# Kernel tuning notes

Measured on AMD Instinct MI355X. Metric: run time of the kernel, lower is better.

Reference implementation:

```python
import jax, jax.numpy as jnp
import numpy as np

DIM = 1024
HEADS = 16
DIM_HEAD = 64
INNER = HEADS * DIM_HEAD
EPS_NORM = 1e-12  # F.normalize eps
LN_EPS = 1e-5     # torch F.layer_norm default eps


def setup_inputs() -> dict:
    key = jax.random.key(0)
    ks = jax.random.split(key, 6)
    x = jax.random.normal(ks[0], (8, 1024, DIM), dtype=jnp.float32)
    ln_gamma = jnp.ones((DIM,), jnp.float32)
    q_gamma = jnp.ones((HEADS, 1, DIM_HEAD), jnp.float32)
    k_gamma = jnp.ones((HEADS, 1, DIM_HEAD), jnp.float32)
    # nn.Linear default init ~ U(-1/sqrt(fan_in), 1/sqrt(fan_in))
    w_qkv = jax.random.uniform(ks[1], (DIM, 3 * INNER), jnp.float32, -1.0, 1.0) / np.sqrt(DIM)
    w_out = jax.random.uniform(ks[2], (INNER, DIM), jnp.float32, -1.0, 1.0) / np.sqrt(INNER)
    return {"x": x, "ln_gamma": ln_gamma, "q_gamma": q_gamma, "k_gamma": k_gamma,
            "w_qkv": w_qkv, "w_out": w_out}


def _layer_norm(x, gamma):
    mu = jnp.mean(x, axis=-1, keepdims=True)
    var = jnp.var(x, axis=-1, keepdims=True)
    return (x - mu) * jax.lax.rsqrt(var + LN_EPS) * gamma  # beta is zeros buffer


def _rms(x, gamma):
    # F.normalize(x, dim=-1) * sqrt(d) * gamma
    n = jnp.linalg.norm(x, axis=-1, keepdims=True)
    normed = x / jnp.maximum(n, EPS_NORM)
    return normed * (DIM_HEAD ** 0.5) * gamma


def reference(x, ln_gamma, q_gamma, k_gamma, w_qkv, w_out):
    b, n, _ = x.shape
    h, d = HEADS, DIM_HEAD
    xn = _layer_norm(x, ln_gamma)
    qkv = xn @ w_qkv  # [b, n, 3*inner]
    q, k, v = jnp.split(qkv, 3, axis=-1)
    # b n (h d) -> b h n d
    to_heads = lambda t: t.reshape(b, n, h, d).transpose(0, 2, 1, 3)
    q, k, v = to_heads(q), to_heads(k), to_heads(v)
    q = _rms(q, q_gamma)
    k = _rms(k, k_gamma)
    dots = jnp.einsum('bhid,bhjd->bhij', q, k)  # no extra scale (scale baked into RMSNorm)
    attn = jax.nn.softmax(dots, axis=-1)
    out = jnp.einsum('bhij,bhjd->bhid', attn, v)
    out = out.transpose(0, 2, 1, 3).reshape(b, n, h * d)
    return out @ w_out
```

## Files before the change

### kernel.cpp

```cpp
#include <hip/hip_runtime.h>
#include <hip/hip_bf16.h>
#include <math.h>

#define DIMX   1024
#define HEADS  16
#define DH     64
#define NB     8
#define NSEQ   1024
#define ROWS   (NB * NSEQ)
#define QKVW   (3 * DIMX)
#define LOG2E  1.44269504088896f

typedef _Float16 half8 __attribute__((ext_vector_type(8)));
typedef _Float16 half4 __attribute__((ext_vector_type(4)));
typedef float floatx4 __attribute__((ext_vector_type(4)));

#define GLD_LDS16(gptr, lptr) __builtin_amdgcn_global_load_lds( \
    (const __attribute__((address_space(1))) void*)(gptr),      \
    (__attribute__((address_space(3))) void*)(lptr), 16, 0, 0)

__device__ __forceinline__ float fexp2(float x) {
#if __has_builtin(__builtin_amdgcn_exp2f)
    return __builtin_amdgcn_exp2f(x);
#else
    return __expf(x * 0.69314718056f);
#endif
}

__global__ __launch_bounds__(256) void ln_kernel(const float* __restrict__ x,
                                                 const float* __restrict__ gamma,
                                                 _Float16* __restrict__ xn) {
    int row = blockIdx.x;
    const float* xr = x + (size_t)row * DIMX;
    _Float16* xo = xn + (size_t)row * DIMX;
    int t = threadIdx.x;

    float4 v = ((const float4*)xr)[t];
    float s  = v.x + v.y + v.z + v.w;
    float ss = v.x*v.x + v.y*v.y + v.z*v.z + v.w*v.w;

    #pragma unroll
    for (int o = 32; o > 0; o >>= 1) {
        s  += __shfl_down(s, o);
        ss += __shfl_down(ss, o);
    }
    __shared__ float sbuf[4], ssbuf[4];
    int lane = t & 63, wid = t >> 6;
    if (lane == 0) { sbuf[wid] = s; ssbuf[wid] = ss; }
    __syncthreads();
    if (t == 0) {
        float a = 0.f, b2 = 0.f;
        for (int i = 0; i < 4; i++) { a += sbuf[i]; b2 += ssbuf[i]; }
        sbuf[0] = a; ssbuf[0] = b2;
    }
    __syncthreads();
    float mean = sbuf[0] * (1.0f / DIMX);
    float var  = ssbuf[0] * (1.0f / DIMX) - mean * mean;
    float rstd = rsqrtf(var + 1e-5f);

    float4 g = ((const float4*)gamma)[t];
    half4 o;
    o.x = (_Float16)((v.x - mean) * rstd * g.x);
    o.y = (_Float16)((v.y - mean) * rstd * g.y);
    o.z = (_Float16)((v.z - mean) * rstd * g.z);
    o.w = (_Float16)((v.w - mean) * rstd * g.w);
    *(half4*)(xo + t * 4) = o;
}

__global__ __launch_bounds__(256) void wtrans2(const float* __restrict__ Wq,
                                               const float* __restrict__ Wo,
                                               _Float16* __restrict__ WqT,
                                               _Float16* __restrict__ WoT) {
    __shared__ float tile[32][33];
    const float* W; _Float16* WT; int N, n0;
    if (blockIdx.x < 96) { W = Wq; WT = WqT; N = QKVW; n0 = blockIdx.x * 32; }
    else                 { W = Wo; WT = WoT; N = DIMX; n0 = (blockIdx.x - 96) * 32; }
    int k0 = blockIdx.y * 32;
    int tx = threadIdx.x & 31, ty = threadIdx.x >> 5;
    #pragma unroll
    for (int i = 0; i < 32; i += 8)
        tile[ty + i][tx] = W[(size_t)(k0 + ty + i) * N + n0 + tx];
    __syncthreads();
    #pragma unroll
    for (int i = 0; i < 32; i += 8)
        WT[(size_t)(n0 + ty + i) * 1024 + k0 + tx] = (_Float16)tile[tx][ty + i];
}

__global__ __launch_bounds__(256) void hgemm_qkv(const _Float16* __restrict__ A,
                                                 const _Float16* __restrict__ BT,
                                                 const float* __restrict__ qg,
                                                 const float* __restrict__ kg,
                                                 _Float16* __restrict__ qf,
                                                 _Float16* __restrict__ kf,
                                                 _Float16* __restrict__ vraw) {
    __shared__ _Float16 As[128 * 64];
    __shared__ _Float16 Bs[128 * 64];
    const int K = DIMX;

    int t = threadIdx.x;
    int wave = t >> 6, lane = t & 63;
    int quad = lane >> 4, l16 = lane & 15;
    int wm = (wave >> 1) * 64;
    int wn = (wave & 1) * 64;
    size_t m0 = (size_t)blockIdx.y * 128, n0 = (size_t)blockIdx.x * 128;

    floatx4 acc[4][4] = {};

    int sr = t >> 3, sg = t & 7;
    int swz = sg ^ (sr & 7);
    const _Float16* ag = A  + (m0 + sr) * (size_t)K + swz * 8;
    const _Float16* bg = BT + (n0 + sr) * (size_t)K + swz * 8;
    char* lA = (char*)As + (t >> 6) * 1024;
    char* lB = (char*)Bs + (t >> 6) * 1024;

    for (int k0 = 0; k0 < K; k0 += 64) {
        #pragma unroll
        for (int i = 0; i < 4; i++) {
            GLD_LDS16(ag + (size_t)(i * 32) * K + k0, lA + i * 4096);
            GLD_LDS16(bg + (size_t)(i * 32) * K + k0, lB + i * 4096);
        }
        __syncthreads();

        half8 af[2][4], bf[2][4];
        #pragma unroll
        for (int kk = 0; kk < 2; kk++) {
            #pragma unroll
            for (int mf = 0; mf < 4; mf++)
                af[kk][mf] = *(const half8*)&As[(wm + mf * 16 + l16) * 64
                                 + (((kk * 4 + quad) ^ (l16 & 7)) * 8)];
            #pragma unroll
            for (int nf = 0; nf < 4; nf++)
                bf[kk][nf] = *(const half8*)&Bs[(wn + nf * 16 + l16) * 64
                                 + (((kk * 4 + quad) ^ (l16 & 7)) * 8)];
        }

        #pragma unroll
        for (int kk = 0; kk < 2; kk++)
            #pragma unroll
            for (int mf = 0; mf < 4; mf++)
                #pragma unroll
                for (int nf = 0; nf < 4; nf++)
                    acc[mf][nf] = __builtin_amdgcn_mfma_f32_16x16x32_f16(
                        bf[kk][nf], af[kk][mf], acc[mf][nf], 0, 0, 0);
        __syncthreads();
    }

    int which = (int)(n0 >> 10);
    int nloc  = ((int)n0 & 1023) + wn;
    int h = nloc >> 6;
    const float* g = (which == 0) ? qg : kg;
    float emul = (which == 0) ? LOG2E : 1.0f;
    _Float16* dstbuf = (which == 0) ? qf : (which == 1) ? kf : vraw;

    #pragma unroll
    for (int mf = 0; mf < 4; mf++) {
        size_t tok = m0 + wm + mf * 16 + l16;
        int b = (int)(tok >> 10), ntk = (int)(tok & 1023);
        _Float16* dst = dstbuf + (((size_t)(b * 16 + h)) * 1024 + ntk) * 64;
        if (which < 2) {
            float ss = 0.f;
            #pragma unroll
            for (int nf = 0; nf < 4; nf++)
                #pragma unroll
                for (int r = 0; r < 4; r++) ss += acc[mf][nf][r] * acc[mf][nf][r];
            ss += __shfl_xor(ss, 16);
            ss += __shfl_xor(ss, 32);
            float scale = 8.0f * emul / fmaxf(sqrtf(ss), 1e-12f);
            #pragma unroll
            for (int nf = 0; nf < 4; nf++) {
                half4 p;
                #pragma unroll
                for (int r = 0; r < 4; r++)
                    p[r] = (_Float16)(acc[mf][nf][r] * scale *
                                      g[h * 64 + nf * 16 + quad * 4 + r]);
                *(half4*)(dst + nf * 16 + quad * 4) = p;
            }
        } else {
            #pragma unroll
            for (int nf = 0; nf < 4; nf++) {
                half4 p;
                #pragma unroll
                for (int r = 0; r < 4; r++) p[r] = (_Float16)acc[mf][nf][r];
                *(half4*)(dst + nf * 16 + quad * 4) = p;
            }
        }
    }
}

__global__ __launch_bounds__(256) void vtrans(const _Float16* __restrict__ vraw,
                                              _Float16* __restrict__ vt) {
    __shared__ _Float16 tile[64][72];
    int blk = blockIdx.x;
    int bh = blk >> 4, nt = blk & 15;
    int t = threadIdx.x;
    int r = t >> 2, cg = t & 3;

    const _Float16* src = vraw + ((size_t)bh * 1024 + nt * 64 + r) * 64 + cg * 16;
    half8 v0 = *(const half8*)src;
    half8 v1 = *(const half8*)(src + 8);
    #pragma unroll
    for (int j = 0; j < 8; j++) tile[cg * 16 + j][r] = v0[j];
    #pragma unroll
    for (int j = 0; j < 8; j++) tile[cg * 16 + 8 + j][r] = v1[j];
    __syncthreads();
    int d = t >> 2, ng = t & 3;
    half8 w0, w1;
    #pragma unroll
    for (int j = 0; j < 8; j++) { w0[j] = tile[d][ng * 16 + j]; w1[j] = tile[d][ng * 16 + 8 + j]; }
    _Float16* vdst = vt + ((size_t)blk * 64 + d) * 64 + ng * 16;
    *(half8*)vdst = w0;
    *(half8*)(vdst + 8) = w1;
}

__global__ __launch_bounds__(256) void flash_kernel(const _Float16* __restrict__ qf,
                                                    const _Float16* __restrict__ kf,
                                                    const _Float16* __restrict__ vt,
                                                    _Float16* __restrict__ obuf) {
    __shared__ _Float16 Ks[64 * 64];
    __shared__ _Float16 VTs[64 * 64];
    __shared__ _Float16 Ps[4][16][68];

    int t = threadIdx.x;
    int wave = t >> 6, lane = t & 63;
    int quad = lane >> 4, l16 = lane & 15;
    int bh = blockIdx.x >> 3, qt = blockIdx.x & 7;

    const _Float16* qb = qf + ((size_t)bh * 1024 + qt * 128) * 64;
    const _Float16* kb = kf + (size_t)bh * 65536;
    const _Float16* vb = vt + (size_t)bh * 65536;

    half8 aq[2][2];
    #pragma unroll
    for (int st = 0; st < 2; st++) {
        const _Float16* qrow = qb + (wave * 32 + st * 16 + l16) * 64;
        aq[st][0] = *(const half8*)(qrow + quad * 8);
        aq[st][1] = *(const half8*)(qrow + 32 + quad * 8);
    }

    floatx4 o[2][4] = {};
    float m_i[2] = {-INFINITY, -INFINITY};
    float l_i[2] = {0.f, 0.f};

    int sr = t >> 3;
    int sg = t & 7;
    int swz = sg ^ (sr & 7);
    char* lK = (char*)Ks  + (t >> 6) * 1024;
    char* lV = (char*)VTs + (t >> 6) * 1024;

    for (int kt = 0; kt < 16; kt++) {
        const _Float16* kbt = kb + (size_t)kt * 64 * 64;
        const _Float16* vbt = vb + (size_t)kt * 64 * 64;
        #pragma unroll
        for (int i = 0; i < 2; i++) {
            GLD_LDS16(kbt + (i * 32 + sr) * 64 + swz * 8, lK + i * 4096);
            GLD_LDS16(vbt + (i * 32 + sr) * 64 + swz * 8, lV + i * 4096);
        }
        __syncthreads();

        #pragma unroll
        for (int st = 0; st < 2; st++) {
            floatx4 sc[4] = {};
            #pragma unroll
            for (int kc = 0; kc < 2; kc++) {
                #pragma unroll
                for (int nf = 0; nf < 4; nf++) {
                    half8 ak = *(const half8*)&Ks[(nf * 16 + l16) * 64
                                    + (((kc * 4 + quad) ^ (l16 & 7)) * 8)];
                    sc[nf] = __builtin_amdgcn_mfma_f32_16x16x32_f16(
                        ak, aq[st][kc], sc[nf], 0, 0, 0);
                }
            }

            float mx = sc[0][0];
            #pragma unroll
            for (int nf = 0; nf < 4; nf++)
                #pragma unroll
                for (int r = 0; r < 4; r++) mx = fmaxf(mx, sc[nf][r]);
            mx = fmaxf(mx, __shfl_xor(mx, 16));
            mx = fmaxf(mx, __shfl_xor(mx, 32));
            if (mx > m_i[st]) {
                float alpha = fexp2(m_i[st] - mx);
                l_i[st] *= alpha;
                #pragma unroll
                for (int nf = 0; nf < 4; nf++) o[st][nf] *= alpha;
                m_i[st] = mx;
            }
            float mcur = m_i[st];
            float psum = 0.f;
            #pragma unroll
            for (int nf = 0; nf < 4; nf++)
                #pragma unroll
                for (int r = 0; r < 4; r++) {
                    float p = fexp2(sc[nf][r] - mcur);
                    sc[nf][r] = p;
                    psum += p;
                }
            l_i[st] += psum;

            #pragma unroll
            for (int nf = 0; nf < 4; nf++) {
                half4 p4;
                #pragma unroll
                for (int r = 0; r < 4; r++) p4[r] = (_Float16)sc[nf][r];
                *(half4*)&Ps[wave][l16][nf * 16 + quad * 4] = p4;
            }

            #pragma unroll
            for (int kc = 0; kc < 2; kc++) {
                half4 p0 = *(const half4*)&Ps[wave][l16][kc * 32 + quad * 8];
                half4 p1 = *(const half4*)&Ps[wave][l16][kc * 32 + quad * 8 + 4];
                half8 bp;
                #pragma unroll
                for (int j = 0; j < 4; j++) { bp[j] = p0[j]; bp[4 + j] = p1[j]; }
                #pragma unroll
                for (int nf = 0; nf < 4; nf++) {
                    half8 av = *(const half8*)&VTs[(nf * 16 + l16) * 64
                                    + (((kc * 4 + quad) ^ (l16 & 7)) * 8)];
                    o[st][nf] = __builtin_amdgcn_mfma_f32_16x16x32_f16(
                        av, bp, o[st][nf], 0, 0, 0);
                }
            }
        }
        __syncthreads();
    }

    int b = bh >> 4, h = bh & 15;
    #pragma unroll
    for (int st = 0; st < 2; st++) {
        float lsum = l_i[st];
        lsum += __shfl_xor(lsum, 16);
        lsum += __shfl_xor(lsum, 32);
        float inv = 1.0f / lsum;
        size_t row = (size_t)b * NSEQ + qt * 128 + wave * 32 + st * 16 + l16;
        #pragma unroll
        for (int nf = 0; nf < 4; nf++) {
            half4 o4;
            #pragma unroll
            for (int r = 0; r < 4; r++) o4[r] = (_Float16)(o[st][nf][r] * inv);
            *(half4*)(obuf + row * 1024 + h * 64 + nf * 16 + quad * 4) = o4;
        }
    }
}

__global__ __launch_bounds__(256) void hgemm_out(const _Float16* __restrict__ A,
                                                 const _Float16* __restrict__ BT,
                                                 float* __restrict__ C) {
    __shared__ _Float16 As[128 * 64];
    __shared__ _Float16 Bs[128 * 64];
    const int K = DIMX, N = DIMX;

    int t = threadIdx.x;
    int wave = t >> 6, lane = t & 63;
    int quad = lane >> 4, l16 = lane & 15;
    int wm = (wave >> 1) * 64, wn = (wave & 1) * 64;
    size_t m0 = (size_t)blockIdx.y * 128, n0 = (size_t)blockIdx.x * 128;

    floatx4 acc[4][4] = {};

    int sr = t >> 3, sg = t & 7;
    int swz = sg ^ (sr & 7);
    const _Float16* ag = A  + (m0 + sr) * (size_t)K + swz * 8;
    const _Float16* bg = BT + (n0 + sr) * (size_t)K + swz * 8;
    char* lA = (char*)As + (t >> 6) * 1024;
    char* lB = (char*)Bs + (t >> 6) * 1024;

    for (int k0 = 0; k0 < K; k0 += 64) {
        #pragma unroll
        for (int i = 0; i < 4; i++) {
            GLD_LDS16(ag + (size_t)(i * 32) * K + k0, lA + i * 4096);
            GLD_LDS16(bg + (size_t)(i * 32) * K + k0, lB + i * 4096);
        }
        __syncthreads();

        half8 af[2][4], bf[2][4];
        #pragma unroll
        for (int kk = 0; kk < 2; kk++) {
            #pragma unroll
            for (int mf = 0; mf < 4; mf++)
                af[kk][mf] = *(const half8*)&As[(wm + mf * 16 + l16) * 64
                                 + (((kk * 4 + quad) ^ (l16 & 7)) * 8)];
            #pragma unroll
            for (int nf = 0; nf < 4; nf++)
                bf[kk][nf] = *(const half8*)&Bs[(wn + nf * 16 + l16) * 64
                                 + (((kk * 4 + quad) ^ (l16 & 7)) * 8)];
        }

        #pragma unroll
        for (int kk = 0; kk < 2; kk++)
            #pragma unroll
            for (int mf = 0; mf < 4; mf++)
                #pragma unroll
                for (int nf = 0; nf < 4; nf++)
                    acc[mf][nf] = __builtin_amdgcn_mfma_f32_16x16x32_f16(
                        bf[kk][nf], af[kk][mf], acc[mf][nf], 0, 0, 0);
        __syncthreads();
    }

    #pragma unroll
    for (int mf = 0; mf < 4; mf++) {
        size_t tok = m0 + wm + mf * 16 + l16;
        #pragma unroll
        for (int nf = 0; nf < 4; nf++)
            *(floatx4*)(C + tok * N + n0 + wn + nf * 16 + quad * 4) = acc[mf][nf];
    }
}

extern "C" void kernel_launch(void* const* d_in, const int* in_sizes, int n_in,
                              void* d_out, int out_size, void* d_ws, size_t ws_size,
                              hipStream_t stream) {
    const float* x     = (const float*)d_in[0];
    const float* ln_g  = (const float*)d_in[1];
    const float* q_g   = (const float*)d_in[2];
    const float* k_g   = (const float*)d_in[3];
    const float* w_qkv = (const float*)d_in[4];
    const float* w_out = (const float*)d_in[5];
    float* out = (float*)d_out;

    char* base = (char*)d_ws;
    _Float16* xn    = (_Float16*)(base);
    _Float16* wqkvT = (_Float16*)(base + (16ull << 20));
    _Float16* woutT = (_Float16*)(base + (22ull << 20));
    _Float16* qf    = (_Float16*)(base + (24ull << 20));
    _Float16* kf    = (_Float16*)(base + (40ull << 20));
    _Float16* vraw  = (_Float16*)(base + (56ull << 20));
    _Float16* vt    = (_Float16*)(base + (72ull << 20));
    _Float16* obuf  = (_Float16*)(base + (88ull << 20));

    ln_kernel<<<ROWS, 256, 0, stream>>>(x, ln_g, xn);

    dim3 gt(128, 32);
    wtrans2<<<gt, 256, 0, stream>>>(w_qkv, w_out, wqkvT, woutT);

    dim3 g1(QKVW / 128, ROWS / 128);
    hgemm_qkv<<<g1, 256, 0, stream>>>(xn, wqkvT, q_g, k_g, qf, kf, vraw);

    vtrans<<<NB * HEADS * (NSEQ / 64), 256, 0, stream>>>(vraw, vt);

    flash_kernel<<<NB * HEADS * (NSEQ / 128), 256, 0, stream>>>(qf, kf, vt, obuf);

    dim3 g2(DIMX / 128, ROWS / 128);
    hgemm_out<<<g2, 256, 0, stream>>>(obuf, woutT, out);
}
```

Measured before the change: 270.6 us.

## Fuse LN with weight transpose, write V transposed in GEMM, double-buffer flash

Merges the layer-norm and weight-transpose kernels into one launch, and removes the separate V transpose kernel by having the QKV GEMM epilogue write V directly in transposed tile layout. The flash attention kernel now double-buffers its K/V tiles in LDS, prefetching the next tile while computing the current one, with one barrier per iteration. It also reorders block indexing so query tiles of the same head are spread across the grid, and adds a launch-bounds occupancy hint. The transposed V stores are strided scalar 2-byte writes, which may be poorly coalesced, and the doubled LDS footprint may limit occupancy.

```diff
diff --git a/kernel.cpp b/kernel.cpp
--- a/kernel.cpp
+++ b/kernel.cpp
@@ -27,63 +27,66 @@
 #endif
 }
 
-__global__ __launch_bounds__(256) void ln_kernel(const float* __restrict__ x,
-                                                 const float* __restrict__ gamma,
-                                                 _Float16* __restrict__ xn) {
-    int row = blockIdx.x;
-    const float* xr = x + (size_t)row * DIMX;
-    _Float16* xo = xn + (size_t)row * DIMX;
+__global__ __launch_bounds__(256) void lnw_kernel(const float* __restrict__ x,
+                                                  const float* __restrict__ gamma,
+                                                  const float* __restrict__ Wq,
+                                                  const float* __restrict__ Wo,
+                                                  _Float16* __restrict__ xn,
+                                                  _Float16* __restrict__ WqT,
+                                                  _Float16* __restrict__ WoT) {
+    __shared__ float tile[32][33];
+    __shared__ float sbuf[4], ssbuf[4];
     int t = threadIdx.x;
 
-    float4 v = ((const float4*)xr)[t];
-    float s  = v.x + v.y + v.z + v.w;
-    float ss = v.x*v.x + v.y*v.y + v.z*v.z + v.w*v.w;
-
-    #pragma unroll
-    for (int o = 32; o > 0; o >>= 1) {
-        s  += __shfl_down(s, o);
-        ss += __shfl_down(ss, o);
-    }
-    __shared__ float sbuf[4], ssbuf[4];
-    int lane = t & 63, wid = t >> 6;
-    if (lane == 0) { sbuf[wid] = s; ssbuf[wid] = ss; }
-    __syncthreads();
-    if (t == 0) {
-        float a = 0.f, b2 = 0.f;
-        for (int i = 0; i < 4; i++) { a += sbuf[i]; b2 += ssbuf[i]; }
-        sbuf[0] = a; ssbuf[0] = b2;
-    }
-    __syncthreads();
-    float mean = sbuf[0] * (1.0f / DIMX);
-    float var  = ssbuf[0] * (1.0f / DIMX) - mean * mean;
-    float rstd = rsqrtf(var + 1e-5f);
-
-    float4 g = ((const float4*)gamma)[t];
-    half4 o;
-    o.x = (_Float16)((v.x - mean) * rstd * g.x);
-    o.y = (_Float16)((v.y - mean) * rstd * g.y);
-    o.z = (_Float16)((v.z - mean) * rstd * g.z);
-    o.w = (_Float16)((v.w - mean) * rstd * g.w);
-    *(half4*)(xo + t * 4) = o;
-}
-
-__global__ __launch_bounds__(256) void wtrans2(const float* __restrict__ Wq,
-                                               const float* __restrict__ Wo,
-                                               _Float16* __restrict__ WqT,
-                                               _Float16* __restrict__ WoT) {
-    __shared__ float tile[32][33];
-    const float* W; _Float16* WT; int N, n0;
-    if (blockIdx.x < 96) { W = Wq; WT = WqT; N = QKVW; n0 = blockIdx.x * 32; }
-    else                 { W = Wo; WT = WoT; N = DIMX; n0 = (blockIdx.x - 96) * 32; }
-    int k0 = blockIdx.y * 32;
-    int tx = threadIdx.x & 31, ty = threadIdx.x >> 5;
-    #pragma unroll
-    for (int i = 0; i < 32; i += 8)
-        tile[ty + i][tx] = W[(size_t)(k0 + ty + i) * N + n0 + tx];
-    __syncthreads();
-    #pragma unroll
-    for (int i = 0; i < 32; i += 8)
-        WT[(size_t)(n0 + ty + i) * 1024 + k0 + tx] = (_Float16)tile[tx][ty + i];
+    if (blockIdx.x < ROWS) {
+        int row = blockIdx.x;
+        const float* xr = x + (size_t)row * DIMX;
+        _Float16* xo = xn + (size_t)row * DIMX;
+
+        float4 v = ((const float4*)xr)[t];
+        float s  = v.x + v.y + v.z + v.w;
+        float ss = v.x*v.x + v.y*v.y + v.z*v.z + v.w*v.w;
+        #pragma unroll
+        for (int o = 32; o > 0; o >>= 1) {
+            s  += __shfl_down(s, o);
+            ss += __shfl_down(ss, o);
+        }
+        int lane = t & 63, wid = t >> 6;
+        if (lane == 0) { sbuf[wid] = s; ssbuf[wid] = ss; }
+        __syncthreads();
+        if (t == 0) {
+            float a = 0.f, b2 = 0.f;
+            for (int i = 0; i < 4; i++) { a += sbuf[i]; b2 += ssbuf[i]; }
+            sbuf[0] = a; ssbuf[0] = b2;
+        }
+        __syncthreads();
+        float mean = sbuf[0] * (1.0f / DIMX);
+        float var  = ssbuf[0] * (1.0f / DIMX) - mean * mean;
+        float rstd = rsqrtf(var + 1e-5f);
+
+        float4 g = ((const float4*)gamma)[t];
+        half4 o;
+        o.x = (_Float16)((v.x - mean) * rstd * g.x);
+        o.y = (_Float16)((v.y - mean) * rstd * g.y);
+        o.z = (_Float16)((v.z - mean) * rstd * g.z);
+        o.w = (_Float16)((v.w - mean) * rstd * g.w);
+        *(half4*)(xo + t * 4) = o;
+    } else {
+        int idx = blockIdx.x - ROWS;
+        int bx = idx & 127, by = idx >> 7;
+        const float* W; _Float16* WT; int N, n0;
+        if (bx < 96) { W = Wq; WT = WqT; N = QKVW; n0 = bx * 32; }
+        else         { W = Wo; WT = WoT; N = DIMX; n0 = (bx - 96) * 32; }
+        int k0 = by * 32;
+        int tx = t & 31, ty = t >> 5;
+        #pragma unroll
+        for (int i = 0; i < 32; i += 8)
+            tile[ty + i][tx] = W[(size_t)(k0 + ty + i) * N + n0 + tx];
+        __syncthreads();
+        #pragma unroll
+        for (int i = 0; i < 32; i += 8)
+            WT[(size_t)(n0 + ty + i) * 1024 + k0 + tx] = (_Float16)tile[tx][ty + i];
+    }
 }
 
 __global__ __launch_bounds__(256) void hgemm_qkv(const _Float16* __restrict__ A,
@@ -92,7 +95,7 @@
                                                  const float* __restrict__ kg,
                                                  _Float16* __restrict__ qf,
                                                  _Float16* __restrict__ kf,
-                                                 _Float16* __restrict__ vraw) {
+                                                 _Float16* __restrict__ vt) {
     __shared__ _Float16 As[128 * 64];
     __shared__ _Float16 Bs[128 * 64];
     const int K = DIMX;
@@ -110,8 +113,8 @@
     int swz = sg ^ (sr & 7);
     const _Float16* ag = A  + (m0 + sr) * (size_t)K + swz * 8;
     const _Float16* bg = BT + (n0 + sr) * (size_t)K + swz * 8;
-    char* lA = (char*)As + (t >> 6) * 1024;
-    char* lB = (char*)Bs + (t >> 6) * 1024;
+    char* lA = (char*)As + wave * 1024;
+    char* lB = (char*)Bs + wave * 1024;
 
     for (int k0 = 0; k0 < K; k0 += 64) {
         #pragma unroll
@@ -148,16 +151,16 @@
     int which = (int)(n0 >> 10);
     int nloc  = ((int)n0 & 1023) + wn;
     int h = nloc >> 6;
-    const float* g = (which == 0) ? qg : kg;
-    float emul = (which == 0) ? LOG2E : 1.0f;
-    _Float16* dstbuf = (which == 0) ? qf : (which == 1) ? kf : vraw;
-
-    #pragma unroll
-    for (int mf = 0; mf < 4; mf++) {
-        size_t tok = m0 + wm + mf * 16 + l16;
-        int b = (int)(tok >> 10), ntk = (int)(tok & 1023);
-        _Float16* dst = dstbuf + (((size_t)(b * 16 + h)) * 1024 + ntk) * 64;
-        if (which < 2) {
+
+    if (which < 2) {
+        const float* g = (which == 0) ? qg : kg;
+        float emul = (which == 0) ? LOG2E : 1.0f;
+        _Float16* dstbuf = (which == 0) ? qf : kf;
+        #pragma unroll
+        for (int mf = 0; mf < 4; mf++) {
+            size_t tok = m0 + wm + mf * 16 + l16;
+            int b = (int)(tok >> 10), ntk = (int)(tok & 1023);
+            _Float16* dst = dstbuf + (((size_t)(b * 16 + h)) * 1024 + ntk) * 64;
             float ss = 0.f;
             #pragma unroll
             for (int nf = 0; nf < 4; nf++)
@@ -175,55 +178,37 @@
                                       g[h * 64 + nf * 16 + quad * 4 + r]);
                 *(half4*)(dst + nf * 16 + quad * 4) = p;
             }
-        } else {
-            #pragma unroll
-            for (int nf = 0; nf < 4; nf++) {
-                half4 p;
-                #pragma unroll
-                for (int r = 0; r < 4; r++) p[r] = (_Float16)acc[mf][nf][r];
-                *(half4*)(dst + nf * 16 + quad * 4) = p;
-            }
-        }
-    }
-}
-
-__global__ __launch_bounds__(256) void vtrans(const _Float16* __restrict__ vraw,
-                                              _Float16* __restrict__ vt) {
-    __shared__ _Float16 tile[64][72];
-    int blk = blockIdx.x;
-    int bh = blk >> 4, nt = blk & 15;
-    int t = threadIdx.x;
-    int r = t >> 2, cg = t & 3;
-
-    const _Float16* src = vraw + ((size_t)bh * 1024 + nt * 64 + r) * 64 + cg * 16;
-    half8 v0 = *(const half8*)src;
-    half8 v1 = *(const half8*)(src + 8);
-    #pragma unroll
-    for (int j = 0; j < 8; j++) tile[cg * 16 + j][r] = v0[j];
-    #pragma unroll
-    for (int j = 0; j < 8; j++) tile[cg * 16 + 8 + j][r] = v1[j];
-    __syncthreads();
-    int d = t >> 2, ng = t & 3;
-    half8 w0, w1;
-    #pragma unroll
-    for (int j = 0; j < 8; j++) { w0[j] = tile[d][ng * 16 + j]; w1[j] = tile[d][ng * 16 + 8 + j]; }
-    _Float16* vdst = vt + ((size_t)blk * 64 + d) * 64 + ng * 16;
-    *(half8*)vdst = w0;
-    *(half8*)(vdst + 8) = w1;
-}
-
-__global__ __launch_bounds__(256) void flash_kernel(const _Float16* __restrict__ qf,
-                                                    const _Float16* __restrict__ kf,
-                                                    const _Float16* __restrict__ vt,
-                                                    _Float16* __restrict__ obuf) {
-    __shared__ _Float16 Ks[64 * 64];
-    __shared__ _Float16 VTs[64 * 64];
+        }
+    } else {
+        #pragma unroll
+        for (int mf = 0; mf < 4; mf++) {
+            size_t tok = m0 + wm + mf * 16 + l16;
+            int b = (int)(tok >> 10), ntk = (int)(tok & 1023);
+            int nt = ntk >> 6;
+            _Float16* vd = vt + ((size_t)((b * 16 + h) * 16 + nt) * 64) * 64
+                              + mf * 16 + l16;
+            #pragma unroll
+            for (int nf = 0; nf < 4; nf++)
+                #pragma unroll
+                for (int r = 0; r < 4; r++)
+                    vd[(size_t)(nf * 16 + quad * 4 + r) * 64] =
+                        (_Float16)acc[mf][nf][r];
+        }
+    }
+}
+
+__global__ __launch_bounds__(256, 3) void flash_kernel(const _Float16* __restrict__ qf,
+                                                       const _Float16* __restrict__ kf,
+                                                       const _Float16* __restrict__ vt,
+                                                       _Float16* __restrict__ obuf) {
+    __shared__ _Float16 Ks[2][64 * 64];
+    __shared__ _Float16 VTs[2][64 * 64];
     __shared__ _Float16 Ps[4][16][68];
 
     int t = threadIdx.x;
     int wave = t >> 6, lane = t & 63;
     int quad = lane >> 4, l16 = lane & 15;
-    int bh = blockIdx.x >> 3, qt = blockIdx.x & 7;
+    int bh = blockIdx.x & 127, qt = blockIdx.x >> 7;
 
     const _Float16* qb = qf + ((size_t)bh * 1024 + qt * 128) * 64;
     const _Float16* kb = kf + (size_t)bh * 65536;
@@ -244,18 +229,28 @@
     int sr = t >> 3;
     int sg = t & 7;
     int swz = sg ^ (sr & 7);
-    char* lK = (char*)Ks  + (t >> 6) * 1024;
-    char* lV = (char*)VTs + (t >> 6) * 1024;
+
+    #pragma unroll
+    for (int i = 0; i < 2; i++) {
+        GLD_LDS16(kb + (i * 32 + sr) * 64 + swz * 8, (char*)Ks[0]  + wave * 1024 + i * 4096);
+        GLD_LDS16(vb + (i * 32 + sr) * 64 + swz * 8, (char*)VTs[0] + wave * 1024 + i * 4096);
+    }
 
     for (int kt = 0; kt < 16; kt++) {
-        const _Float16* kbt = kb + (size_t)kt * 64 * 64;
-        const _Float16* vbt = vb + (size_t)kt * 64 * 64;
-        #pragma unroll
-        for (int i = 0; i < 2; i++) {
-            GLD_LDS16(kbt + (i * 32 + sr) * 64 + swz * 8, lK + i * 4096);
-            GLD_LDS16(vbt + (i * 32 + sr) * 64 + swz * 8, lV + i * 4096);
-        }
-        __syncthreads();
+        int cur = kt & 1;
+        __syncthreads();
+
+        if (kt < 15) {
+            const _Float16* kn = kb + (size_t)(kt + 1) * 4096;
+            const _Float16* vn = vb + (size_t)(kt + 1) * 4096;
+            #pragma unroll
+            for (int i = 0; i < 2; i++) {
+                GLD_LDS16(kn + (i * 32 + sr) * 64 + swz * 8,
+                          (char*)Ks[cur ^ 1]  + wave * 1024 + i * 4096);
+                GLD_LDS16(vn + (i * 32 + sr) * 64 + swz * 8,
+                          (char*)VTs[cur ^ 1] + wave * 1024 + i * 4096);
+            }
+        }
 
         #pragma unroll
         for (int st = 0; st < 2; st++) {
@@ -264,7 +259,7 @@
             for (int kc = 0; kc < 2; kc++) {
                 #pragma unroll
                 for (int nf = 0; nf < 4; nf++) {
-                    half8 ak = *(const half8*)&Ks[(nf * 16 + l16) * 64
+                    half8 ak = *(const half8*)&Ks[cur][(nf * 16 + l16) * 64
                                     + (((kc * 4 + quad) ^ (l16 & 7)) * 8)];
                     sc[nf] = __builtin_amdgcn_mfma_f32_16x16x32_f16(
                         ak, aq[st][kc], sc[nf], 0, 0, 0);
@@ -314,14 +309,13 @@
                 for (int j = 0; j < 4; j++) { bp[j] = p0[j]; bp[4 + j] = p1[j]; }
                 #pragma unroll
                 for (int nf = 0; nf < 4; nf++) {
-                    half8 av = *(const half8*)&VTs[(nf * 16 + l16) * 64
+                    half8 av = *(const half8*)&VTs[cur][(nf * 16 + l16) * 64
                                     + (((kc * 4 + quad) ^ (l16 & 7)) * 8)];
                     o[st][nf] = __builtin_amdgcn_mfma_f32_16x16x32_f16(
                         av, bp, o[st][nf], 0, 0, 0);
                 }
             }
         }
-        __syncthreads();
     }
 
     int b = bh >> 4, h = bh & 15;
@@ -361,8 +355,8 @@
     int swz = sg ^ (sr & 7);
     const _Float16* ag = A  + (m0 + sr) * (size_t)K + swz * 8;
     const _Float16* bg = BT + (n0 + sr) * (size_t)K + swz * 8;
-    char* lA = (char*)As + (t >> 6) * 1024;
-    char* lB = (char*)Bs + (t >> 6) * 1024;
+    char* lA = (char*)As + wave * 1024;
+    char* lB = (char*)Bs + wave * 1024;
 
     for (int k0 = 0; k0 < K; k0 += 64) {
         #pragma unroll
@@ -422,19 +416,14 @@
     _Float16* woutT = (_Float16*)(base + (22ull << 20));
     _Float16* qf    = (_Float16*)(base + (24ull << 20));
     _Float16* kf    = (_Float16*)(base + (40ull << 20));
-    _Float16* vraw  = (_Float16*)(base + (56ull << 20));
-    _Float16* vt    = (_Float16*)(base + (72ull << 20));
-    _Float16* obuf  = (_Float16*)(base + (88ull << 20));
-
-    ln_kernel<<<ROWS, 256, 0, stream>>>(x, ln_g, xn);
-
-    dim3 gt(128, 32);
-    wtrans2<<<gt, 256, 0, stream>>>(w_qkv, w_out, wqkvT, woutT);
+    _Float16* vt    = (_Float16*)(base + (56ull << 20));
+    _Float16* obuf  = (_Float16*)(base + (72ull << 20));
+
+    lnw_kernel<<<ROWS + 4096, 256, 0, stream>>>(x, ln_g, w_qkv, w_out,
+                                                xn, wqkvT, woutT);
 
     dim3 g1(QKVW / 128, ROWS / 128);
-    hgemm_qkv<<<g1, 256, 0, stream>>>(xn, wqkvT, q_g, k_g, qf, kf, vraw);
-
-    vtrans<<<NB * HEADS * (NSEQ / 64), 256, 0, stream>>>(vraw, vt);
+    hgemm_qkv<<<g1, 256, 0, stream>>>(xn, wqkvT, q_g, k_g, qf, kf, vt);
 
     flash_kernel<<<NB * HEADS * (NSEQ / 128), 256, 0, stream>>>(qf, kf, vt, obuf);
 
```

Measured after the change: 250.0 us. 1.08x faster.
